# Kernel tuning notes

Hardware: AMD Instinct MI355X
Metric: run time of the kernel (lower is better)

## Reference

```python
import jax, jax.numpy as jnp
import numpy as np

T, N = 20, 32768          # seq_length, numNodes
D_IN, D_EMB, D_H, D_OUT = 2, 64, 128, 5


def setup_inputs() -> dict:
    key = jax.random.key(0)
    ks = jax.random.split(key, 12)
    s = 0.05
    return {
        "nodes": jax.random.normal(ks[0], (T, N, D_IN), jnp.float32),
        "present_mask": jax.random.randint(ks[1], (T, N), 0, 2).astype(bool),
        "hidden_states": jax.random.normal(ks[2], (N, D_H), jnp.float32),
        "cell_states": jax.random.normal(ks[3], (N, D_H), jnp.float32),
        "W_embed": jax.random.normal(ks[4], (D_IN, D_EMB), jnp.float32) * s,
        "b_embed": jnp.zeros((D_EMB,), jnp.float32),
        "W_ih": jax.random.normal(ks[5], (D_EMB, 4 * D_H), jnp.float32) * s,
        "b_ih": jnp.zeros((4 * D_H,), jnp.float32),
        "W_hh": jax.random.normal(ks[6], (D_H, 4 * D_H), jnp.float32) * s,
        "b_hh": jnp.zeros((4 * D_H,), jnp.float32),
        "W_out": jax.random.normal(ks[7], (D_H, D_OUT), jnp.float32) * s,
        "b_out": jnp.zeros((D_OUT,), jnp.float32),
    }


def reference(nodes, present_mask, hidden_states, cell_states,
              W_embed, b_embed, W_ih, b_ih, W_hh, b_hh, W_out, b_out):
    # Per-frame: gather present nodes -> embed+ReLU (dropout=eval identity)
    # -> LSTMCell -> scatter h/c/output back. Gather+scatter is expressed as
    # a masked update, which is mathematically identical.
    def step(carry, frame):
        h, c = carry
        x, mask = frame                      # x: [N,2], mask: [N]
        emb = jax.nn.relu(x @ W_embed + b_embed)              # [N,Demb]
        gates = emb @ W_ih + b_ih + h @ W_hh + b_hh           # [N,4H]
        i, f, g, o = jnp.split(gates, 4, axis=-1)             # torch order
        i, f, o = jax.nn.sigmoid(i), jax.nn.sigmoid(f), jax.nn.sigmoid(o)
        g = jnp.tanh(g)
        c_new = f * c + i * g
        h_new = o * jnp.tanh(c_new)
        m = mask[:, None]
        h = jnp.where(m, h_new, h)
        c = jnp.where(m, c_new, c)
        out = jnp.where(m, h_new @ W_out + b_out, 0.0)        # absent -> zeros
        return (h, c), out

    (h_fin, c_fin), outputs = jax.lax.scan(
        step, (hidden_states, cell_states), (nodes, present_mask))
    return outputs, h_fin, c_fin                              # [T,N,5],[N,H],[N,H]
```

## Files before the change

### kernel.cpp

```cpp
#include <hip/hip_runtime.h>
#include <cstddef>


typedef __attribute__((ext_vector_type(8))) short  s16x8;
typedef __attribute__((ext_vector_type(4))) float  f32x4;

namespace {
constexpr int T_STEPS = 20;
constexpr int NN      = 32768;
constexpr int D_EMB   = 64;
constexpr int D_H     = 128;
constexpr int D_OUT   = 5;
constexpr int G4      = 512;
constexpr int MT      = 64;
constexpr int BLOCK   = 512;
constexpr int GRID    = NN / MT;
constexpr int WP_ELEMS   = 8 * 4 * 6 * 64 * 8;
constexpr int WOUT_ELEMS = 4 * 64 * 8;
constexpr size_t OFF_H = (size_t)T_STEPS * NN * D_OUT;
constexpr size_t OFF_C = OFF_H + (size_t)NN * D_H;
}

__device__ __forceinline__ unsigned short f2bf(float x) {
    unsigned u = __float_as_uint(x);
    u = (u + 0x7FFFu + ((u >> 16) & 1u)) >> 16;
    return (unsigned short)u;
}
__device__ __forceinline__ float bf2f(unsigned short h) {
    return __uint_as_float(((unsigned)h) << 16);
}
__device__ __forceinline__ float sigf(float x) {
    return __builtin_amdgcn_rcpf(1.0f + __expf(-x));
}
__device__ __forceinline__ float tanhf_fast(float x) {
    return fmaf(-2.0f, __builtin_amdgcn_rcpf(1.0f + __expf(2.0f * x)), 1.0f);
}

__global__ void prepack_kernel(const float* __restrict__ W_ih,
                               const float* __restrict__ b_ih,
                               const float* __restrict__ W_hh,
                               const float* __restrict__ b_hh,
                               const float* __restrict__ W_out,
                               unsigned short* __restrict__ Wp,
                               unsigned short* __restrict__ WoutF,
                               float* __restrict__ b_sum) {
    int idx = blockIdx.x * blockDim.x + threadIdx.x;
    if (idx < WP_ELEMS) {
        int j    = idx & 7;
        int L    = (idx >> 3) & 63;
        int rest = idx >> 9;
        int kb   = rest % 6;
        int gw   = rest / 6;
        int g    = gw & 3, w = gw >> 2;
        int k    = kb * 32 + (L >> 4) * 8 + j;
        int col  = g * D_H + w * 16 + (L & 15);
        float v  = (k < D_EMB) ? W_ih[k * G4 + col] : W_hh[(k - D_EMB) * G4 + col];
        Wp[idx] = f2bf(v);
    } else if (idx < WP_ELEMS + WOUT_ELEMS) {
        int i2 = idx - WP_ELEMS;
        int j = i2 & 7, L = (i2 >> 3) & 63, kb2 = i2 >> 9;
        int k = kb2 * 32 + (L >> 4) * 8 + j;
        int n = L & 15;
        WoutF[i2] = (n < D_OUT) ? f2bf(W_out[k * D_OUT + n]) : (unsigned short)0;
    }
    if (idx < G4) b_sum[idx] = b_ih[idx] + b_hh[idx];
}

__global__ __launch_bounds__(BLOCK, 2) void vlstm_kernel(
    const float* __restrict__ nodes,
    const int*   __restrict__ mask,
    const float* __restrict__ h0,
    const float* __restrict__ c0,
    const float* __restrict__ W_embed,
    const float* __restrict__ b_embed,
    const float* __restrict__ b_out,
    const unsigned short* __restrict__ Wp,
    const unsigned short* __restrict__ WoutF,
    const float* __restrict__ b_sum,
    float* __restrict__ out)
{
    __shared__ __align__(16) unsigned short A[24 * 64 * 8];
    __shared__ __align__(16) float st_out[MT * D_OUT];
    __shared__ float We_s[2 * D_EMB];
    __shared__ float be_s[D_EMB];
    __shared__ int   msk_s[2][MT];

    const int tid  = threadIdx.x;
    const int wave = tid >> 6;
    const int L    = tid & 63;
    const int quad = L >> 4;
    const int l15  = L & 15;
    const int n_base = blockIdx.x * MT;

    const unsigned short* wbase = Wp + (size_t)wave * (4 * 6 * 64 * 8);
    s16x8 Bf[4][6];
    #pragma unroll
    for (int g = 0; g < 4; g++)
        #pragma unroll
        for (int kb = 0; kb < 6; kb++)
            Bf[g][kb] = *(const s16x8*)(wbase + ((g * 6 + kb) * 64 + L) * 8);
    s16x8 WoF[4];
    #pragma unroll
    for (int kb2 = 0; kb2 < 4; kb2++)
        WoF[kb2] = *(const s16x8*)(WoutF + ((kb2 * 64) + L) * 8);

    float bias[4];
    #pragma unroll
    for (int g = 0; g < 4; g++) bias[g] = b_sum[g * D_H + wave * 16 + l15];
    const float bo = (l15 < D_OUT) ? b_out[l15] : 0.0f;

    for (int i = tid; i < 3 * D_EMB; i += BLOCK) {
        if (i < 2 * D_EMB) We_s[i] = W_embed[i];
        else               be_s[i - 2 * D_EMB] = b_embed[i - 2 * D_EMB];
    }
    for (int i = tid; i < MT * D_H; i += BLOCK) {
        int node = i >> 7, u = i & 127;
        int k = D_EMB + u;
        int idx = (((node >> 4) * 6 + (k >> 5)) * 64 + ((k >> 3) & 3) * 16 + (node & 15)) * 8 + (k & 7);
        A[idx] = f2bf(h0[(size_t)(n_base + node) * D_H + u]);
    }
    const int u_lane = wave * 16 + l15;
    float c[4][4];
    #pragma unroll
    for (int rt = 0; rt < 4; rt++)
        #pragma unroll
        for (int r = 0; r < 4; r++) {
            int m = rt * 16 + quad * 4 + r;
            c[rt][r] = c0[(size_t)(n_base + m) * D_H + u_lane];
        }
    __syncthreads();

    const int node_e = tid >> 3;
    const int eb     = tid & 7;

    {
        const float2* xp = (const float2*)(nodes + ((size_t)0 * NN + n_base + node_e) * 2);
        float2 x = *xp;
        s16x8 ev;
        #pragma unroll
        for (int j = 0; j < 8; j++) {
            int e = eb * 8 + j;
            float v = fmaf(x.x, We_s[e], fmaf(x.y, We_s[D_EMB + e], be_s[e]));
            ev[j] = (short)f2bf(fmaxf(v, 0.0f));
        }
        int idx = (((node_e >> 4) * 6 + (eb >> 2)) * 64 + (eb & 3) * 16 + (node_e & 15)) * 8;
        *(s16x8*)(A + idx) = ev;
        if (tid < MT) msk_s[0][tid] = mask[(size_t)0 * NN + n_base + tid];
    }
    __syncthreads();

    for (int t = 0; t < T_STEPS; t++) {
        f32x4 acc[4][4];
        #pragma unroll
        for (int rt = 0; rt < 4; rt++)
            #pragma unroll
            for (int g = 0; g < 4; g++)
                acc[rt][g] = (f32x4){bias[g], bias[g], bias[g], bias[g]};
        #pragma unroll
        for (int kb = 0; kb < 6; kb++) {
            #pragma unroll
            for (int rt = 0; rt < 4; rt++) {
                s16x8 af = *(const s16x8*)(A + ((rt * 6 + kb) * 64 + L) * 8);
                #pragma unroll
                for (int g = 0; g < 4; g++)
                    acc[rt][g] = __builtin_amdgcn_mfma_f32_16x16x32_bf16(
                        af, Bf[g][kb], acc[rt][g], 0, 0, 0);
            }
        }

        unsigned mbits = 0;
        unsigned short hbf[4][4];
        #pragma unroll
        for (int rt = 0; rt < 4; rt++)
            #pragma unroll
            for (int r = 0; r < 4; r++) {
                int m = rt * 16 + quad * 4 + r;
                int mval = msk_s[t & 1][m];
                float gi = sigf(acc[rt][0][r]);
                float gf = sigf(acc[rt][1][r]);
                float gg = tanhf_fast(acc[rt][2][r]);
                float go = sigf(acc[rt][3][r]);
                float cn = fmaf(gf, c[rt][r], gi * gg);
                float hv = go * tanhf_fast(cn);
                if (mval) { c[rt][r] = cn; mbits |= 1u << (rt * 4 + r); }
                hbf[rt][r] = f2bf(hv);
            }
        __syncthreads();

        if (t > 0 && tid < MT * D_OUT)
            out[((size_t)(t - 1) * NN + n_base) * D_OUT + tid] = st_out[tid];

        {
            int kb_u = 2 + (u_lane >> 5);
            int fl   = ((u_lane >> 3) & 3) * 16 + quad * 4;
            int j_u  = u_lane & 7;
            #pragma unroll
            for (int rt = 0; rt < 4; rt++)
                #pragma unroll
                for (int r = 0; r < 4; r++)
                    if ((mbits >> (rt * 4 + r)) & 1u)
                        A[((rt * 6 + kb_u) * 64 + fl + r) * 8 + j_u] = hbf[rt][r];
        }
        if (t + 1 < T_STEPS) {
            const float2* xp = (const float2*)(nodes + ((size_t)(t + 1) * NN + n_base + node_e) * 2);
            float2 x = *xp;
            s16x8 ev;
            #pragma unroll
            for (int j = 0; j < 8; j++) {
                int e = eb * 8 + j;
                float v = fmaf(x.x, We_s[e], fmaf(x.y, We_s[D_EMB + e], be_s[e]));
                ev[j] = (short)f2bf(fmaxf(v, 0.0f));
            }
            int idx = (((node_e >> 4) * 6 + (eb >> 2)) * 64 + (eb & 3) * 16 + (node_e & 15)) * 8;
            *(s16x8*)(A + idx) = ev;
            if (tid < MT) msk_s[(t + 1) & 1][tid] = mask[(size_t)(t + 1) * NN + n_base + tid];
        }
        __syncthreads();

        if (wave < 4) {
            const int rt = wave;
            f32x4 ao = (f32x4){0.0f, 0.0f, 0.0f, 0.0f};
            #pragma unroll
            for (int kb2 = 0; kb2 < 4; kb2++) {
                s16x8 af = *(const s16x8*)(A + ((rt * 6 + 2 + kb2) * 64 + L) * 8);
                ao = __builtin_amdgcn_mfma_f32_16x16x32_bf16(af, WoF[kb2], ao, 0, 0, 0);
            }
            if (l15 < D_OUT) {
                #pragma unroll
                for (int r = 0; r < 4; r++) {
                    int node = rt * 16 + quad * 4 + r;
                    int mv = msk_s[t & 1][node];
                    st_out[node * D_OUT + l15] = mv ? (ao[r] + bo) : 0.0f;
                }
            }
        }
    }

    __syncthreads();
    if (tid < MT * D_OUT)
        out[((size_t)(T_STEPS - 1) * NN + n_base) * D_OUT + tid] = st_out[tid];

    for (int i = tid; i < MT * D_H; i += BLOCK) {
        int node = i >> 7, u = i & 127;
        int k = D_EMB + u;
        int idx = (((node >> 4) * 6 + (k >> 5)) * 64 + ((k >> 3) & 3) * 16 + (node & 15)) * 8 + (k & 7);
        out[OFF_H + (size_t)(n_base + node) * D_H + u] = bf2f(A[idx]);
    }
    #pragma unroll
    for (int rt = 0; rt < 4; rt++)
        #pragma unroll
        for (int r = 0; r < 4; r++) {
            int m = rt * 16 + quad * 4 + r;
            out[OFF_C + (size_t)(n_base + m) * D_H + u_lane] = c[rt][r];
        }
}

extern "C" void kernel_launch(void* const* d_in, const int* in_sizes, int n_in,
                              void* d_out, int out_size, void* d_ws, size_t ws_size,
                              hipStream_t stream) {
    const float* nodes   = (const float*)d_in[0];
    const int*   mask    = (const int*)  d_in[1];
    const float* h0      = (const float*)d_in[2];
    const float* c0      = (const float*)d_in[3];
    const float* W_embed = (const float*)d_in[4];
    const float* b_embed = (const float*)d_in[5];
    const float* W_ih    = (const float*)d_in[6];
    const float* b_ih    = (const float*)d_in[7];
    const float* W_hh    = (const float*)d_in[8];
    const float* b_hh    = (const float*)d_in[9];
    const float* W_out   = (const float*)d_in[10];
    const float* b_out   = (const float*)d_in[11];
    float* out = (float*)d_out;

    unsigned short* Wp    = (unsigned short*)d_ws;
    unsigned short* WoutF = Wp + WP_ELEMS;
    float*          b_sum = (float*)(WoutF + WOUT_ELEMS);

    prepack_kernel<<<(WP_ELEMS + WOUT_ELEMS + 255) / 256, 256, 0, stream>>>(
        W_ih, b_ih, W_hh, b_hh, W_out, Wp, WoutF, b_sum);

    vlstm_kernel<<<GRID, BLOCK, 0, stream>>>(
        nodes, mask, h0, c0, W_embed, b_embed, b_out, Wp, WoutF, b_sum, out);
}
```

Measured before the change: 331.3 us.

## Double-buffer LDS activation tile to cut one barrier per LSTM step

The single shared A tile becomes two ping-pong buffers, so each step reads the current buffer and writes h and the next embedding into the other, leaving one __syncthreads per step instead of two. The output projection for step k-1 and the global store for step k-2 are moved to the start of step k, overlapping with the gate matmul. Next-step inputs and the mask are loaded early into registers to hide global latency, and h is now kept in registers and written in full each step. In exchange, LDS use roughly doubles, which may cut occupancy at 2 blocks per CU, and register pressure goes up.

```diff
diff --git a/kernel.cpp b/kernel.cpp
--- a/kernel.cpp
+++ b/kernel.cpp
@@ -17,6 +17,7 @@
 constexpr int GRID    = NN / MT;
 constexpr int WP_ELEMS   = 8 * 4 * 6 * 64 * 8;
 constexpr int WOUT_ELEMS = 4 * 64 * 8;
+constexpr int AELEMS  = 24 * 64 * 8;
 constexpr size_t OFF_H = (size_t)T_STEPS * NN * D_OUT;
 constexpr size_t OFF_C = OFF_H + (size_t)NN * D_H;
 }
@@ -79,8 +80,8 @@
     const float* __restrict__ b_sum,
     float* __restrict__ out)
 {
-    __shared__ __align__(16) unsigned short A[24 * 64 * 8];
-    __shared__ __align__(16) float st_out[MT * D_OUT];
+    __shared__ __align__(16) unsigned short Abuf[2][AELEMS];
+    __shared__ __align__(16) float st_out[2][MT * D_OUT];
     __shared__ float We_s[2 * D_EMB];
     __shared__ float be_s[D_EMB];
     __shared__ int   msk_s[2][MT];
@@ -117,18 +118,19 @@
         int node = i >> 7, u = i & 127;
         int k = D_EMB + u;
         int idx = (((node >> 4) * 6 + (k >> 5)) * 64 + ((k >> 3) & 3) * 16 + (node & 15)) * 8 + (k & 7);
-        A[idx] = f2bf(h0[(size_t)(n_base + node) * D_H + u]);
+        Abuf[0][idx] = f2bf(h0[(size_t)(n_base + node) * D_H + u]);
     }
     const int u_lane = wave * 16 + l15;
     float c[4][4];
+    unsigned short hcur[4][4];
     #pragma unroll
     for (int rt = 0; rt < 4; rt++)
         #pragma unroll
         for (int r = 0; r < 4; r++) {
             int m = rt * 16 + quad * 4 + r;
-            c[rt][r] = c0[(size_t)(n_base + m) * D_H + u_lane];
-        }
-    __syncthreads();
+            c[rt][r]    = c0[(size_t)(n_base + m) * D_H + u_lane];
+            hcur[rt][r] = f2bf(h0[(size_t)(n_base + m) * D_H + u_lane]);
+        }
 
     const int node_e = tid >> 3;
     const int eb     = tid & 7;
@@ -144,12 +146,51 @@
             ev[j] = (short)f2bf(fmaxf(v, 0.0f));
         }
         int idx = (((node_e >> 4) * 6 + (eb >> 2)) * 64 + (eb & 3) * 16 + (node_e & 15)) * 8;
-        *(s16x8*)(A + idx) = ev;
+        *(s16x8*)(Abuf[0] + idx) = ev;
         if (tid < MT) msk_s[0][tid] = mask[(size_t)0 * NN + n_base + tid];
     }
     __syncthreads();
 
-    for (int t = 0; t < T_STEPS; t++) {
+    const int kb_u = 2 + (u_lane >> 5);
+    const int fl   = ((u_lane >> 3) & 3) * 16 + quad * 4;
+    const int j_u  = u_lane & 7;
+
+    unsigned mprev = 0;
+
+    for (int k = 0; k < T_STEPS; k++) {
+        const int p = k & 1;
+        const unsigned short* Ac = Abuf[p];
+        unsigned short*       An = Abuf[1 - p];
+        const bool has_next = (k + 1 < T_STEPS);
+
+        float2 xv = {0.0f, 0.0f};
+        int mpf = 0;
+        if (has_next) {
+            xv = *(const float2*)(nodes + ((size_t)(k + 1) * NN + n_base + node_e) * 2);
+            if (tid < MT) mpf = mask[(size_t)(k + 1) * NN + n_base + tid];
+        }
+
+        if (k > 0 && wave < 4) {
+            const int rt = wave;
+            f32x4 ao = (f32x4){0.0f, 0.0f, 0.0f, 0.0f};
+            #pragma unroll
+            for (int kb2 = 0; kb2 < 4; kb2++) {
+                s16x8 af = *(const s16x8*)(Ac + ((rt * 6 + 2 + kb2) * 64 + L) * 8);
+                ao = __builtin_amdgcn_mfma_f32_16x16x32_bf16(af, WoF[kb2], ao, 0, 0, 0);
+            }
+            if (l15 < D_OUT) {
+                #pragma unroll
+                for (int r = 0; r < 4; r++) {
+                    int node = rt * 16 + quad * 4 + r;
+                    st_out[1 - p][node * D_OUT + l15] =
+                        ((mprev >> (rt * 4 + r)) & 1u) ? (ao[r] + bo) : 0.0f;
+                }
+            }
+        }
+
+        if (k > 1 && tid < MT * D_OUT)
+            out[((size_t)(k - 2) * NN + n_base) * D_OUT + tid] = st_out[p][tid];
+
         f32x4 acc[4][4];
         #pragma unroll
         for (int rt = 0; rt < 4; rt++)
@@ -160,7 +201,7 @@
         for (int kb = 0; kb < 6; kb++) {
             #pragma unroll
             for (int rt = 0; rt < 4; rt++) {
-                s16x8 af = *(const s16x8*)(A + ((rt * 6 + kb) * 64 + L) * 8);
+                s16x8 af = *(const s16x8*)(Ac + ((rt * 6 + kb) * 64 + L) * 8);
                 #pragma unroll
                 for (int g = 0; g < 4; g++)
                     acc[rt][g] = __builtin_amdgcn_mfma_f32_16x16x32_bf16(
@@ -169,82 +210,84 @@
         }
 
         unsigned mbits = 0;
-        unsigned short hbf[4][4];
         #pragma unroll
         for (int rt = 0; rt < 4; rt++)
             #pragma unroll
             for (int r = 0; r < 4; r++) {
                 int m = rt * 16 + quad * 4 + r;
-                int mval = msk_s[t & 1][m];
+                int mval = msk_s[p][m];
                 float gi = sigf(acc[rt][0][r]);
                 float gf = sigf(acc[rt][1][r]);
                 float gg = tanhf_fast(acc[rt][2][r]);
                 float go = sigf(acc[rt][3][r]);
                 float cn = fmaf(gf, c[rt][r], gi * gg);
                 float hv = go * tanhf_fast(cn);
-                if (mval) { c[rt][r] = cn; mbits |= 1u << (rt * 4 + r); }
-                hbf[rt][r] = f2bf(hv);
-            }
-        __syncthreads();
-
-        if (t > 0 && tid < MT * D_OUT)
-            out[((size_t)(t - 1) * NN + n_base) * D_OUT + tid] = st_out[tid];
-
-        {
-            int kb_u = 2 + (u_lane >> 5);
-            int fl   = ((u_lane >> 3) & 3) * 16 + quad * 4;
-            int j_u  = u_lane & 7;
-            #pragma unroll
-            for (int rt = 0; rt < 4; rt++)
-                #pragma unroll
-                for (int r = 0; r < 4; r++)
-                    if ((mbits >> (rt * 4 + r)) & 1u)
-                        A[((rt * 6 + kb_u) * 64 + fl + r) * 8 + j_u] = hbf[rt][r];
-        }
-        if (t + 1 < T_STEPS) {
-            const float2* xp = (const float2*)(nodes + ((size_t)(t + 1) * NN + n_base + node_e) * 2);
-            float2 x = *xp;
+                if (mval) {
+                    c[rt][r]    = cn;
+                    hcur[rt][r] = f2bf(hv);
+                    mbits |= 1u << (rt * 4 + r);
+                }
+            }
+        mprev = mbits;
+
+        #pragma unroll
+        for (int rt = 0; rt < 4; rt++)
+            #pragma unroll
+            for (int r = 0; r < 4; r++)
+                An[((rt * 6 + kb_u) * 64 + fl + r) * 8 + j_u] = hcur[rt][r];
+
+        if (has_next) {
             s16x8 ev;
             #pragma unroll
             for (int j = 0; j < 8; j++) {
                 int e = eb * 8 + j;
-                float v = fmaf(x.x, We_s[e], fmaf(x.y, We_s[D_EMB + e], be_s[e]));
+                float v = fmaf(xv.x, We_s[e], fmaf(xv.y, We_s[D_EMB + e], be_s[e]));
                 ev[j] = (short)f2bf(fmaxf(v, 0.0f));
             }
             int idx = (((node_e >> 4) * 6 + (eb >> 2)) * 64 + (eb & 3) * 16 + (node_e & 15)) * 8;
-            *(s16x8*)(A + idx) = ev;
-            if (tid < MT) msk_s[(t + 1) & 1][tid] = mask[(size_t)(t + 1) * NN + n_base + tid];
-        }
+            *(s16x8*)(An + idx) = ev;
+            if (tid < MT) msk_s[1 - p][tid] = mpf;
+        }
+
         __syncthreads();
-
+    }
+
+    {
+        const unsigned short* Ah = Abuf[T_STEPS & 1];
         if (wave < 4) {
             const int rt = wave;
             f32x4 ao = (f32x4){0.0f, 0.0f, 0.0f, 0.0f};
             #pragma unroll
             for (int kb2 = 0; kb2 < 4; kb2++) {
-                s16x8 af = *(const s16x8*)(A + ((rt * 6 + 2 + kb2) * 64 + L) * 8);
+                s16x8 af = *(const s16x8*)(Ah + ((rt * 6 + 2 + kb2) * 64 + L) * 8);
                 ao = __builtin_amdgcn_mfma_f32_16x16x32_bf16(af, WoF[kb2], ao, 0, 0, 0);
             }
             if (l15 < D_OUT) {
                 #pragma unroll
                 for (int r = 0; r < 4; r++) {
                     int node = rt * 16 + quad * 4 + r;
-                    int mv = msk_s[t & 1][node];
-                    st_out[node * D_OUT + l15] = mv ? (ao[r] + bo) : 0.0f;
+                    st_out[(T_STEPS - 1) & 1][node * D_OUT + l15] =
+                        ((mprev >> (rt * 4 + r)) & 1u) ? (ao[r] + bo) : 0.0f;
                 }
             }
         }
-    }
-
+        if (tid < MT * D_OUT)
+            out[((size_t)(T_STEPS - 2) * NN + n_base) * D_OUT + tid] =
+                st_out[(T_STEPS - 2) & 1][tid];
+    }
     __syncthreads();
     if (tid < MT * D_OUT)
-        out[((size_t)(T_STEPS - 1) * NN + n_base) * D_OUT + tid] = st_out[tid];
-
-    for (int i = tid; i < MT * D_H; i += BLOCK) {
-        int node = i >> 7, u = i & 127;
-        int k = D_EMB + u;
-        int idx = (((node >> 4) * 6 + (k >> 5)) * 64 + ((k >> 3) & 3) * 16 + (node & 15)) * 8 + (k & 7);
-        out[OFF_H + (size_t)(n_base + node) * D_H + u] = bf2f(A[idx]);
+        out[((size_t)(T_STEPS - 1) * NN + n_base) * D_OUT + tid] =
+            st_out[(T_STEPS - 1) & 1][tid];
+
+    {
+        const unsigned short* Ah = Abuf[T_STEPS & 1];
+        for (int i = tid; i < MT * D_H; i += BLOCK) {
+            int node = i >> 7, u = i & 127;
+            int kk = D_EMB + u;
+            int idx = (((node >> 4) * 6 + (kk >> 5)) * 64 + ((kk >> 3) & 3) * 16 + (node & 15)) * 8 + (kk & 7);
+            out[OFF_H + (size_t)(n_base + node) * D_H + u] = bf2f(Ah[idx]);
+        }
     }
     #pragma unroll
     for (int rt = 0; rt < 4; rt++)
```

Result: slower. 401.6 us (+21.2%).

## Double node tile per block and prefetch next-step inputs before MFMA

Applied to the files above, without the earlier changes.

Doubles the node tile per block from 64 to 128, so each wave reuses its register-resident gate weights across 8 row tiles, processed in two halves. Next-frame node coordinates and mask are loaded into registers before the gate MFMAs to hide global latency. The output projection weights move from registers to LDS so all 8 waves can do the output MFMA, and the output mask is taken from the per-lane mask bits. bf16 packing now uses paired conversions. The risks are a grid of only 256 blocks, which lowers occupancy, and higher register pressure that could cause spills.

```diff
diff --git a/kernel.cpp b/kernel.cpp
--- a/kernel.cpp
+++ b/kernel.cpp
@@ -1,4 +1,5 @@
 #include <hip/hip_runtime.h>
+#include <hip/hip_bf16.h>
 #include <cstddef>
 
 
@@ -12,11 +13,12 @@
 constexpr int D_H     = 128;
 constexpr int D_OUT   = 5;
 constexpr int G4      = 512;
-constexpr int MT      = 64;
+constexpr int MT      = 128;
 constexpr int BLOCK   = 512;
 constexpr int GRID    = NN / MT;
 constexpr int WP_ELEMS   = 8 * 4 * 6 * 64 * 8;
 constexpr int WOUT_ELEMS = 4 * 64 * 8;
+constexpr int AELEMS  = 8 * 6 * 64 * 8;
 constexpr size_t OFF_H = (size_t)T_STEPS * NN * D_OUT;
 constexpr size_t OFF_C = OFF_H + (size_t)NN * D_H;
 }
@@ -28,6 +30,10 @@
 }
 __device__ __forceinline__ float bf2f(unsigned short h) {
     return __uint_as_float(((unsigned)h) << 16);
+}
+__device__ __forceinline__ unsigned pk2bf(float lo, float hi) {
+    __hip_bfloat162 p = __float22bfloat162_rn(make_float2(lo, hi));
+    return *(unsigned*)&p;
 }
 __device__ __forceinline__ float sigf(float x) {
     return __builtin_amdgcn_rcpf(1.0f + __expf(-x));
@@ -79,7 +85,8 @@
     const float* __restrict__ b_sum,
     float* __restrict__ out)
 {
-    __shared__ __align__(16) unsigned short A[24 * 64 * 8];
+    __shared__ __align__(16) unsigned short A[AELEMS];
+    __shared__ __align__(16) unsigned short WoF_s[WOUT_ELEMS];
     __shared__ __align__(16) float st_out[MT * D_OUT];
     __shared__ float We_s[2 * D_EMB];
     __shared__ float be_s[D_EMB];
@@ -99,16 +106,14 @@
         #pragma unroll
         for (int kb = 0; kb < 6; kb++)
             Bf[g][kb] = *(const s16x8*)(wbase + ((g * 6 + kb) * 64 + L) * 8);
-    s16x8 WoF[4];
-    #pragma unroll
-    for (int kb2 = 0; kb2 < 4; kb2++)
-        WoF[kb2] = *(const s16x8*)(WoutF + ((kb2 * 64) + L) * 8);
 
     float bias[4];
     #pragma unroll
     for (int g = 0; g < 4; g++) bias[g] = b_sum[g * D_H + wave * 16 + l15];
     const float bo = (l15 < D_OUT) ? b_out[l15] : 0.0f;
 
+    for (int i = tid; i < WOUT_ELEMS / 8; i += BLOCK)
+        *(s16x8*)(WoF_s + i * 8) = *(const s16x8*)(WoutF + i * 8);
     for (int i = tid; i < 3 * D_EMB; i += BLOCK) {
         if (i < 2 * D_EMB) We_s[i] = W_embed[i];
         else               be_s[i - 2 * D_EMB] = b_embed[i - 2 * D_EMB];
@@ -120,125 +125,152 @@
         A[idx] = f2bf(h0[(size_t)(n_base + node) * D_H + u]);
     }
     const int u_lane = wave * 16 + l15;
-    float c[4][4];
+    float c[8][4];
     #pragma unroll
-    for (int rt = 0; rt < 4; rt++)
+    for (int rt = 0; rt < 8; rt++)
         #pragma unroll
         for (int r = 0; r < 4; r++) {
             int m = rt * 16 + quad * 4 + r;
             c[rt][r] = c0[(size_t)(n_base + m) * D_H + u_lane];
         }
-    __syncthreads();
 
     const int node_e = tid >> 3;
     const int eb     = tid & 7;
 
     {
-        const float2* xp = (const float2*)(nodes + ((size_t)0 * NN + n_base + node_e) * 2);
-        float2 x = *xp;
-        s16x8 ev;
-        #pragma unroll
-        for (int j = 0; j < 8; j++) {
-            int e = eb * 8 + j;
-            float v = fmaf(x.x, We_s[e], fmaf(x.y, We_s[D_EMB + e], be_s[e]));
-            ev[j] = (short)f2bf(fmaxf(v, 0.0f));
-        }
-        int idx = (((node_e >> 4) * 6 + (eb >> 2)) * 64 + (eb & 3) * 16 + (node_e & 15)) * 8;
-        *(s16x8*)(A + idx) = ev;
+        #pragma unroll
+        for (int h = 0; h < 2; h++) {
+            int node = node_e + 64 * h;
+            float2 x = *(const float2*)(nodes + ((size_t)0 * NN + n_base + node) * 2);
+            union { s16x8 v; unsigned u[4]; } ev;
+            #pragma unroll
+            for (int jp = 0; jp < 4; jp++) {
+                int e = eb * 8 + jp * 2;
+                float v0 = fmaf(x.x, We_s[e],     fmaf(x.y, We_s[D_EMB + e],     be_s[e]));
+                float v1 = fmaf(x.x, We_s[e + 1], fmaf(x.y, We_s[D_EMB + e + 1], be_s[e + 1]));
+                ev.u[jp] = pk2bf(fmaxf(v0, 0.0f), fmaxf(v1, 0.0f));
+            }
+            int idx = (((node >> 4) * 6 + (eb >> 2)) * 64 + (eb & 3) * 16 + (node & 15)) * 8;
+            *(s16x8*)(A + idx) = ev.v;
+        }
         if (tid < MT) msk_s[0][tid] = mask[(size_t)0 * NN + n_base + tid];
     }
     __syncthreads();
 
+    const int kb_u = 2 + (u_lane >> 5);
+    const int fl   = ((u_lane >> 3) & 3) * 16 + quad * 4;
+    const int j_u  = u_lane & 7;
+
     for (int t = 0; t < T_STEPS; t++) {
-        f32x4 acc[4][4];
-        #pragma unroll
-        for (int rt = 0; rt < 4; rt++)
-            #pragma unroll
-            for (int g = 0; g < 4; g++)
-                acc[rt][g] = (f32x4){bias[g], bias[g], bias[g], bias[g]};
-        #pragma unroll
-        for (int kb = 0; kb < 6; kb++) {
-            #pragma unroll
-            for (int rt = 0; rt < 4; rt++) {
-                s16x8 af = *(const s16x8*)(A + ((rt * 6 + kb) * 64 + L) * 8);
+        const int p = t & 1;
+        const bool has_next = (t + 1 < T_STEPS);
+
+        float2 xv[2] = {{0.f, 0.f}, {0.f, 0.f}};
+        int mpf = 0;
+        if (has_next) {
+            xv[0] = *(const float2*)(nodes + ((size_t)(t + 1) * NN + n_base + node_e) * 2);
+            xv[1] = *(const float2*)(nodes + ((size_t)(t + 1) * NN + n_base + node_e + 64) * 2);
+            if (tid < MT) mpf = mask[(size_t)(t + 1) * NN + n_base + tid];
+        }
+
+        unsigned mbits = 0;
+        unsigned hpk[8][2];
+        #pragma unroll
+        for (int half = 0; half < 2; half++) {
+            f32x4 acc[4][4];
+            #pragma unroll
+            for (int q = 0; q < 4; q++)
                 #pragma unroll
                 for (int g = 0; g < 4; g++)
-                    acc[rt][g] = __builtin_amdgcn_mfma_f32_16x16x32_bf16(
-                        af, Bf[g][kb], acc[rt][g], 0, 0, 0);
-            }
-        }
-
-        unsigned mbits = 0;
-        unsigned short hbf[4][4];
-        #pragma unroll
-        for (int rt = 0; rt < 4; rt++)
-            #pragma unroll
-            for (int r = 0; r < 4; r++) {
-                int m = rt * 16 + quad * 4 + r;
-                int mval = msk_s[t & 1][m];
-                float gi = sigf(acc[rt][0][r]);
-                float gf = sigf(acc[rt][1][r]);
-                float gg = tanhf_fast(acc[rt][2][r]);
-                float go = sigf(acc[rt][3][r]);
-                float cn = fmaf(gf, c[rt][r], gi * gg);
-                float hv = go * tanhf_fast(cn);
-                if (mval) { c[rt][r] = cn; mbits |= 1u << (rt * 4 + r); }
-                hbf[rt][r] = f2bf(hv);
-            }
+                    acc[q][g] = (f32x4){bias[g], bias[g], bias[g], bias[g]};
+            #pragma unroll
+            for (int kb = 0; kb < 6; kb++) {
+                #pragma unroll
+                for (int q = 0; q < 4; q++) {
+                    int rt = half * 4 + q;
+                    s16x8 af = *(const s16x8*)(A + ((rt * 6 + kb) * 64 + L) * 8);
+                    #pragma unroll
+                    for (int g = 0; g < 4; g++)
+                        acc[q][g] = __builtin_amdgcn_mfma_f32_16x16x32_bf16(
+                            af, Bf[g][kb], acc[q][g], 0, 0, 0);
+                }
+            }
+            #pragma unroll
+            for (int q = 0; q < 4; q++) {
+                int rt = half * 4 + q;
+                float hv[4];
+                #pragma unroll
+                for (int r = 0; r < 4; r++) {
+                    int m = rt * 16 + quad * 4 + r;
+                    int mval = msk_s[p][m];
+                    float gi = sigf(acc[q][0][r]);
+                    float gf = sigf(acc[q][1][r]);
+                    float gg = tanhf_fast(acc[q][2][r]);
+                    float go = sigf(acc[q][3][r]);
+                    float cn = fmaf(gf, c[rt][r], gi * gg);
+                    hv[r] = go * tanhf_fast(cn);
+                    if (mval) { c[rt][r] = cn; mbits |= 1u << (rt * 4 + r); }
+                }
+                hpk[rt][0] = pk2bf(hv[0], hv[1]);
+                hpk[rt][1] = pk2bf(hv[2], hv[3]);
+            }
+        }
         __syncthreads();
 
-        if (t > 0 && tid < MT * D_OUT)
-            out[((size_t)(t - 1) * NN + n_base) * D_OUT + tid] = st_out[tid];
+        if (t > 0)
+            for (int i = tid; i < MT * D_OUT; i += BLOCK)
+                out[((size_t)(t - 1) * NN + n_base) * D_OUT + i] = st_out[i];
+
+        #pragma unroll
+        for (int rt = 0; rt < 8; rt++)
+            #pragma unroll
+            for (int r = 0; r < 4; r++)
+                if ((mbits >> (rt * 4 + r)) & 1u)
+                    A[((rt * 6 + kb_u) * 64 + fl + r) * 8 + j_u] =
+                        (unsigned short)(hpk[rt][r >> 1] >> ((r & 1) * 16));
+
+        if (has_next) {
+            #pragma unroll
+            for (int h = 0; h < 2; h++) {
+                int node = node_e + 64 * h;
+                union { s16x8 v; unsigned u[4]; } ev;
+                #pragma unroll
+                for (int jp = 0; jp < 4; jp++) {
+                    int e = eb * 8 + jp * 2;
+                    float v0 = fmaf(xv[h].x, We_s[e],     fmaf(xv[h].y, We_s[D_EMB + e],     be_s[e]));
+                    float v1 = fmaf(xv[h].x, We_s[e + 1], fmaf(xv[h].y, We_s[D_EMB + e + 1], be_s[e + 1]));
+                    ev.u[jp] = pk2bf(fmaxf(v0, 0.0f), fmaxf(v1, 0.0f));
+                }
+                int idx = (((node >> 4) * 6 + (eb >> 2)) * 64 + (eb & 3) * 16 + (node & 15)) * 8;
+                *(s16x8*)(A + idx) = ev.v;
+            }
+            if (tid < MT) msk_s[1 - p][tid] = mpf;
+        }
+        __syncthreads();
 
         {
-            int kb_u = 2 + (u_lane >> 5);
-            int fl   = ((u_lane >> 3) & 3) * 16 + quad * 4;
-            int j_u  = u_lane & 7;
-            #pragma unroll
-            for (int rt = 0; rt < 4; rt++)
-                #pragma unroll
-                for (int r = 0; r < 4; r++)
-                    if ((mbits >> (rt * 4 + r)) & 1u)
-                        A[((rt * 6 + kb_u) * 64 + fl + r) * 8 + j_u] = hbf[rt][r];
-        }
-        if (t + 1 < T_STEPS) {
-            const float2* xp = (const float2*)(nodes + ((size_t)(t + 1) * NN + n_base + node_e) * 2);
-            float2 x = *xp;
-            s16x8 ev;
-            #pragma unroll
-            for (int j = 0; j < 8; j++) {
-                int e = eb * 8 + j;
-                float v = fmaf(x.x, We_s[e], fmaf(x.y, We_s[D_EMB + e], be_s[e]));
-                ev[j] = (short)f2bf(fmaxf(v, 0.0f));
-            }
-            int idx = (((node_e >> 4) * 6 + (eb >> 2)) * 64 + (eb & 3) * 16 + (node_e & 15)) * 8;
-            *(s16x8*)(A + idx) = ev;
-            if (tid < MT) msk_s[(t + 1) & 1][tid] = mask[(size_t)(t + 1) * NN + n_base + tid];
-        }
-        __syncthreads();
-
-        if (wave < 4) {
             const int rt = wave;
             f32x4 ao = (f32x4){0.0f, 0.0f, 0.0f, 0.0f};
             #pragma unroll
             for (int kb2 = 0; kb2 < 4; kb2++) {
                 s16x8 af = *(const s16x8*)(A + ((rt * 6 + 2 + kb2) * 64 + L) * 8);
-                ao = __builtin_amdgcn_mfma_f32_16x16x32_bf16(af, WoF[kb2], ao, 0, 0, 0);
+                s16x8 wf = *(const s16x8*)(WoF_s + (kb2 * 64 + L) * 8);
+                ao = __builtin_amdgcn_mfma_f32_16x16x32_bf16(af, wf, ao, 0, 0, 0);
             }
             if (l15 < D_OUT) {
                 #pragma unroll
                 for (int r = 0; r < 4; r++) {
                     int node = rt * 16 + quad * 4 + r;
-                    int mv = msk_s[t & 1][node];
-                    st_out[node * D_OUT + l15] = mv ? (ao[r] + bo) : 0.0f;
+                    st_out[node * D_OUT + l15] =
+                        ((mbits >> (rt * 4 + r)) & 1u) ? (ao[r] + bo) : 0.0f;
                 }
             }
         }
     }
 
     __syncthreads();
-    if (tid < MT * D_OUT)
-        out[((size_t)(T_STEPS - 1) * NN + n_base) * D_OUT + tid] = st_out[tid];
+    for (int i = tid; i < MT * D_OUT; i += BLOCK)
+        out[((size_t)(T_STEPS - 1) * NN + n_base) * D_OUT + i] = st_out[i];
 
     for (int i = tid; i < MT * D_H; i += BLOCK) {
         int node = i >> 7, u = i & 127;
@@ -247,7 +279,7 @@
         out[OFF_H + (size_t)(n_base + node) * D_H + u] = bf2f(A[idx]);
     }
     #pragma unroll
-    for (int rt = 0; rt < 4; rt++)
+    for (int rt = 0; rt < 8; rt++)
         #pragma unroll
         for (int r = 0; r < 4; r++) {
             int m = rt * 16 + quad * 4 + r;
```

Measured after the change: 550.7 us. 66.2% more time.

## Split LSTM gates across wave pairs with LDS exchange, double block size

Applied to the files above, without the earlier changes.

Doubles the block to 1024 threads (16 waves). Each pair of waves now shares a 16-unit slice, with each wave computing two of the four gates. The odd wave applies the g/o activations and passes them as packed bf16 through a new LDS exchange buffer. The even wave finishes the cell update and writes h back. This halves per-wave MFMA and register work so more waves can overlap, and next-step input loads are now issued before the matmul. In exchange it adds a synchronized LDS round trip, bf16 rounding of the g/o activations, and heavier LDS use that may limit occupancy.

```diff
diff --git a/kernel.cpp b/kernel.cpp
--- a/kernel.cpp
+++ b/kernel.cpp
@@ -1,4 +1,5 @@
 #include <hip/hip_runtime.h>
+#include <hip/hip_bf16.h>
 #include <cstddef>
 
 
@@ -13,10 +14,11 @@
 constexpr int D_OUT   = 5;
 constexpr int G4      = 512;
 constexpr int MT      = 64;
-constexpr int BLOCK   = 512;
+constexpr int BLOCK   = 1024;
 constexpr int GRID    = NN / MT;
-constexpr int WP_ELEMS   = 8 * 4 * 6 * 64 * 8;
+constexpr int WP_ELEMS   = 16 * 2 * 6 * 64 * 8;
 constexpr int WOUT_ELEMS = 4 * 64 * 8;
+constexpr int AELEMS  = 24 * 64 * 8;
 constexpr size_t OFF_H = (size_t)T_STEPS * NN * D_OUT;
 constexpr size_t OFF_C = OFF_H + (size_t)NN * D_H;
 }
@@ -28,6 +30,10 @@
 }
 __device__ __forceinline__ float bf2f(unsigned short h) {
     return __uint_as_float(((unsigned)h) << 16);
+}
+__device__ __forceinline__ unsigned pk2bf(float lo, float hi) {
+    __hip_bfloat162 p = __float22bfloat162_rn(make_float2(lo, hi));
+    return *(unsigned*)&p;
 }
 __device__ __forceinline__ float sigf(float x) {
     return __builtin_amdgcn_rcpf(1.0f + __expf(-x));
@@ -50,10 +56,12 @@
         int L    = (idx >> 3) & 63;
         int rest = idx >> 9;
         int kb   = rest % 6;
-        int gw   = rest / 6;
-        int g    = gw & 3, w = gw >> 2;
+        int wg   = rest / 6;
+        int gg   = wg & 1, w = wg >> 1;
+        int ug   = w >> 1;
+        int gate = (w & 1) * 2 + gg;
         int k    = kb * 32 + (L >> 4) * 8 + j;
-        int col  = g * D_H + w * 16 + (L & 15);
+        int col  = gate * D_H + ug * 16 + (L & 15);
         float v  = (k < D_EMB) ? W_ih[k * G4 + col] : W_hh[(k - D_EMB) * G4 + col];
         Wp[idx] = f2bf(v);
     } else if (idx < WP_ELEMS + WOUT_ELEMS) {
@@ -66,7 +74,7 @@
     if (idx < G4) b_sum[idx] = b_ih[idx] + b_hh[idx];
 }
 
-__global__ __launch_bounds__(BLOCK, 2) void vlstm_kernel(
+__global__ __launch_bounds__(BLOCK, 4) void vlstm_kernel(
     const float* __restrict__ nodes,
     const int*   __restrict__ mask,
     const float* __restrict__ h0,
@@ -79,7 +87,8 @@
     const float* __restrict__ b_sum,
     float* __restrict__ out)
 {
-    __shared__ __align__(16) unsigned short A[24 * 64 * 8];
+    __shared__ __align__(16) unsigned short A[AELEMS];
+    __shared__ __align__(16) unsigned Xex[8 * 64 * 17];
     __shared__ __align__(16) float st_out[MT * D_OUT];
     __shared__ float We_s[2 * D_EMB];
     __shared__ float be_s[D_EMB];
@@ -87,26 +96,34 @@
 
     const int tid  = threadIdx.x;
     const int wave = tid >> 6;
+    const int aodd = wave & 1;
+    const int ug   = wave >> 1;
     const int L    = tid & 63;
     const int quad = L >> 4;
     const int l15  = L & 15;
     const int n_base = blockIdx.x * MT;
-
-    const unsigned short* wbase = Wp + (size_t)wave * (4 * 6 * 64 * 8);
-    s16x8 Bf[4][6];
+    const int u_lane = ug * 16 + l15;
+
+    const unsigned short* wbase = Wp + (size_t)wave * (2 * 6 * 64 * 8);
+    s16x8 Bf[2][6];
     #pragma unroll
-    for (int g = 0; g < 4; g++)
+    for (int gg = 0; gg < 2; gg++)
         #pragma unroll
         for (int kb = 0; kb < 6; kb++)
-            Bf[g][kb] = *(const s16x8*)(wbase + ((g * 6 + kb) * 64 + L) * 8);
+            Bf[gg][kb] = *(const s16x8*)(wbase + ((gg * 6 + kb) * 64 + L) * 8);
+
+    float bias[2];
+    #pragma unroll
+    for (int gg = 0; gg < 2; gg++)
+        bias[gg] = b_sum[(aodd * 2 + gg) * D_H + u_lane];
+
     s16x8 WoF[4];
-    #pragma unroll
-    for (int kb2 = 0; kb2 < 4; kb2++)
-        WoF[kb2] = *(const s16x8*)(WoutF + ((kb2 * 64) + L) * 8);
-
-    float bias[4];
-    #pragma unroll
-    for (int g = 0; g < 4; g++) bias[g] = b_sum[g * D_H + wave * 16 + l15];
+    const int do_oproj = (aodd == 1 && ug < 4);
+    if (do_oproj) {
+        #pragma unroll
+        for (int kb2 = 0; kb2 < 4; kb2++)
+            WoF[kb2] = *(const s16x8*)(WoutF + ((kb2 * 64) + L) * 8);
+    }
     const float bo = (l15 < D_OUT) ? b_out[l15] : 0.0f;
 
     for (int i = tid; i < 3 * D_EMB; i += BLOCK) {
@@ -119,106 +136,124 @@
         int idx = (((node >> 4) * 6 + (k >> 5)) * 64 + ((k >> 3) & 3) * 16 + (node & 15)) * 8 + (k & 7);
         A[idx] = f2bf(h0[(size_t)(n_base + node) * D_H + u]);
     }
-    const int u_lane = wave * 16 + l15;
     float c[4][4];
-    #pragma unroll
-    for (int rt = 0; rt < 4; rt++)
-        #pragma unroll
-        for (int r = 0; r < 4; r++) {
-            int m = rt * 16 + quad * 4 + r;
-            c[rt][r] = c0[(size_t)(n_base + m) * D_H + u_lane];
-        }
+    if (aodd == 0) {
+        #pragma unroll
+        for (int rt = 0; rt < 4; rt++)
+            #pragma unroll
+            for (int r = 0; r < 4; r++) {
+                int m = rt * 16 + quad * 4 + r;
+                c[rt][r] = c0[(size_t)(n_base + m) * D_H + u_lane];
+            }
+    }
+
+    const int node_e = tid >> 4;
+    const int eb     = tid & 15;
+
+    {
+        float2 x = *(const float2*)(nodes + ((size_t)0 * NN + n_base + node_e) * 2);
+        int e0 = eb * 4;
+        float v0 = fmaf(x.x, We_s[e0],     fmaf(x.y, We_s[D_EMB + e0],     be_s[e0]));
+        float v1 = fmaf(x.x, We_s[e0 + 1], fmaf(x.y, We_s[D_EMB + e0 + 1], be_s[e0 + 1]));
+        float v2 = fmaf(x.x, We_s[e0 + 2], fmaf(x.y, We_s[D_EMB + e0 + 2], be_s[e0 + 2]));
+        float v3 = fmaf(x.x, We_s[e0 + 3], fmaf(x.y, We_s[D_EMB + e0 + 3], be_s[e0 + 3]));
+        uint2 pk;
+        pk.x = pk2bf(fmaxf(v0, 0.0f), fmaxf(v1, 0.0f));
+        pk.y = pk2bf(fmaxf(v2, 0.0f), fmaxf(v3, 0.0f));
+        int idx = (((node_e >> 4) * 6 + (e0 >> 5)) * 64 + ((e0 >> 3) & 3) * 16 + (node_e & 15)) * 8 + (e0 & 7);
+        *(uint2*)(A + idx) = pk;
+        if (tid < MT) msk_s[0][tid] = mask[(size_t)0 * NN + n_base + tid];
+    }
     __syncthreads();
 
-    const int node_e = tid >> 3;
-    const int eb     = tid & 7;
-
-    {
-        const float2* xp = (const float2*)(nodes + ((size_t)0 * NN + n_base + node_e) * 2);
-        float2 x = *xp;
-        s16x8 ev;
-        #pragma unroll
-        for (int j = 0; j < 8; j++) {
-            int e = eb * 8 + j;
-            float v = fmaf(x.x, We_s[e], fmaf(x.y, We_s[D_EMB + e], be_s[e]));
-            ev[j] = (short)f2bf(fmaxf(v, 0.0f));
-        }
-        int idx = (((node_e >> 4) * 6 + (eb >> 2)) * 64 + (eb & 3) * 16 + (node_e & 15)) * 8;
-        *(s16x8*)(A + idx) = ev;
-        if (tid < MT) msk_s[0][tid] = mask[(size_t)0 * NN + n_base + tid];
-    }
-    __syncthreads();
+    const int kb_u = 2 + (u_lane >> 5);
+    const int fl   = ((u_lane >> 3) & 3) * 16 + quad * 4;
+    const int j_u  = u_lane & 7;
+    const int xbase = (ug * 64 + L) * 17;
 
     for (int t = 0; t < T_STEPS; t++) {
-        f32x4 acc[4][4];
+        const int p = t & 1;
+        const bool has_next = (t + 1 < T_STEPS);
+
+        float2 xv = {0.0f, 0.0f};
+        int mpf = 0;
+        if (has_next) {
+            xv = *(const float2*)(nodes + ((size_t)(t + 1) * NN + n_base + node_e) * 2);
+            if (tid < MT) mpf = mask[(size_t)(t + 1) * NN + n_base + tid];
+        }
+
+        f32x4 acc[4][2];
         #pragma unroll
         for (int rt = 0; rt < 4; rt++)
             #pragma unroll
-            for (int g = 0; g < 4; g++)
-                acc[rt][g] = (f32x4){bias[g], bias[g], bias[g], bias[g]};
+            for (int gg = 0; gg < 2; gg++)
+                acc[rt][gg] = (f32x4){bias[gg], bias[gg], bias[gg], bias[gg]};
         #pragma unroll
         for (int kb = 0; kb < 6; kb++) {
             #pragma unroll
             for (int rt = 0; rt < 4; rt++) {
                 s16x8 af = *(const s16x8*)(A + ((rt * 6 + kb) * 64 + L) * 8);
-                #pragma unroll
-                for (int g = 0; g < 4; g++)
-                    acc[rt][g] = __builtin_amdgcn_mfma_f32_16x16x32_bf16(
-                        af, Bf[g][kb], acc[rt][g], 0, 0, 0);
-            }
-        }
-
-        unsigned mbits = 0;
-        unsigned short hbf[4][4];
-        #pragma unroll
-        for (int rt = 0; rt < 4; rt++)
-            #pragma unroll
-            for (int r = 0; r < 4; r++) {
-                int m = rt * 16 + quad * 4 + r;
-                int mval = msk_s[t & 1][m];
-                float gi = sigf(acc[rt][0][r]);
-                float gf = sigf(acc[rt][1][r]);
-                float gg = tanhf_fast(acc[rt][2][r]);
-                float go = sigf(acc[rt][3][r]);
-                float cn = fmaf(gf, c[rt][r], gi * gg);
-                float hv = go * tanhf_fast(cn);
-                if (mval) { c[rt][r] = cn; mbits |= 1u << (rt * 4 + r); }
-                hbf[rt][r] = f2bf(hv);
-            }
+                acc[rt][0] = __builtin_amdgcn_mfma_f32_16x16x32_bf16(af, Bf[0][kb], acc[rt][0], 0, 0, 0);
+                acc[rt][1] = __builtin_amdgcn_mfma_f32_16x16x32_bf16(af, Bf[1][kb], acc[rt][1], 0, 0, 0);
+            }
+        }
+
+        if (aodd == 1) {
+            #pragma unroll
+            for (int rt = 0; rt < 4; rt++) {
+                uint4 xw;
+                xw.x = pk2bf(tanhf_fast(acc[rt][0][0]), sigf(acc[rt][1][0]));
+                xw.y = pk2bf(tanhf_fast(acc[rt][0][1]), sigf(acc[rt][1][1]));
+                xw.z = pk2bf(tanhf_fast(acc[rt][0][2]), sigf(acc[rt][1][2]));
+                xw.w = pk2bf(tanhf_fast(acc[rt][0][3]), sigf(acc[rt][1][3]));
+                *(uint4*)(Xex + xbase + rt * 4) = xw;
+            }
+        }
         __syncthreads();
 
         if (t > 0 && tid < MT * D_OUT)
             out[((size_t)(t - 1) * NN + n_base) * D_OUT + tid] = st_out[tid];
 
-        {
-            int kb_u = 2 + (u_lane >> 5);
-            int fl   = ((u_lane >> 3) & 3) * 16 + quad * 4;
-            int j_u  = u_lane & 7;
-            #pragma unroll
-            for (int rt = 0; rt < 4; rt++)
+        if (aodd == 0) {
+            #pragma unroll
+            for (int rt = 0; rt < 4; rt++) {
+                uint4 xr = *(const uint4*)(Xex + xbase + rt * 4);
+                unsigned xa[4] = {xr.x, xr.y, xr.z, xr.w};
                 #pragma unroll
-                for (int r = 0; r < 4; r++)
-                    if ((mbits >> (rt * 4 + r)) & 1u)
-                        A[((rt * 6 + kb_u) * 64 + fl + r) * 8 + j_u] = hbf[rt][r];
-        }
-        if (t + 1 < T_STEPS) {
-            const float2* xp = (const float2*)(nodes + ((size_t)(t + 1) * NN + n_base + node_e) * 2);
-            float2 x = *xp;
-            s16x8 ev;
-            #pragma unroll
-            for (int j = 0; j < 8; j++) {
-                int e = eb * 8 + j;
-                float v = fmaf(x.x, We_s[e], fmaf(x.y, We_s[D_EMB + e], be_s[e]));
-                ev[j] = (short)f2bf(fmaxf(v, 0.0f));
-            }
-            int idx = (((node_e >> 4) * 6 + (eb >> 2)) * 64 + (eb & 3) * 16 + (node_e & 15)) * 8;
-            *(s16x8*)(A + idx) = ev;
-            if (tid < MT) msk_s[(t + 1) & 1][tid] = mask[(size_t)(t + 1) * NN + n_base + tid];
+                for (int r = 0; r < 4; r++) {
+                    int m = rt * 16 + quad * 4 + r;
+                    int mval = msk_s[p][m];
+                    float si = sigf(acc[rt][0][r]);
+                    float sf = sigf(acc[rt][1][r]);
+                    float tg = bf2f((unsigned short)(xa[r] & 0xFFFFu));
+                    float so = bf2f((unsigned short)(xa[r] >> 16));
+                    float cn = fmaf(sf, c[rt][r], si * tg);
+                    float hv = so * tanhf_fast(cn);
+                    if (mval) {
+                        c[rt][r] = cn;
+                        A[((rt * 6 + kb_u) * 64 + fl + r) * 8 + j_u] = f2bf(hv);
+                    }
+                }
+            }
+        }
+
+        if (has_next) {
+            int e0 = eb * 4;
+            float v0 = fmaf(xv.x, We_s[e0],     fmaf(xv.y, We_s[D_EMB + e0],     be_s[e0]));
+            float v1 = fmaf(xv.x, We_s[e0 + 1], fmaf(xv.y, We_s[D_EMB + e0 + 1], be_s[e0 + 1]));
+            float v2 = fmaf(xv.x, We_s[e0 + 2], fmaf(xv.y, We_s[D_EMB + e0 + 2], be_s[e0 + 2]));
+            float v3 = fmaf(xv.x, We_s[e0 + 3], fmaf(xv.y, We_s[D_EMB + e0 + 3], be_s[e0 + 3]));
+            uint2 pk;
+            pk.x = pk2bf(fmaxf(v0, 0.0f), fmaxf(v1, 0.0f));
+            pk.y = pk2bf(fmaxf(v2, 0.0f), fmaxf(v3, 0.0f));
+            int idx = (((node_e >> 4) * 6 + (e0 >> 5)) * 64 + ((e0 >> 3) & 3) * 16 + (node_e & 15)) * 8 + (e0 & 7);
+            *(uint2*)(A + idx) = pk;
+            if (tid < MT) msk_s[1 - p][tid] = mpf;
         }
         __syncthreads();
 
-        if (wave < 4) {
-            const int rt = wave;
+        if (do_oproj) {
+            const int rt = ug;
             f32x4 ao = (f32x4){0.0f, 0.0f, 0.0f, 0.0f};
             #pragma unroll
             for (int kb2 = 0; kb2 < 4; kb2++) {
@@ -229,8 +264,8 @@
                 #pragma unroll
                 for (int r = 0; r < 4; r++) {
                     int node = rt * 16 + quad * 4 + r;
-                    int mv = msk_s[t & 1][node];
-                    st_out[node * D_OUT + l15] = mv ? (ao[r] + bo) : 0.0f;
+                    st_out[node * D_OUT + l15] =
+                        msk_s[p][node] ? (ao[r] + bo) : 0.0f;
                 }
             }
         }
@@ -246,13 +281,15 @@
         int idx = (((node >> 4) * 6 + (k >> 5)) * 64 + ((k >> 3) & 3) * 16 + (node & 15)) * 8 + (k & 7);
         out[OFF_H + (size_t)(n_base + node) * D_H + u] = bf2f(A[idx]);
     }
-    #pragma unroll
-    for (int rt = 0; rt < 4; rt++)
-        #pragma unroll
-        for (int r = 0; r < 4; r++) {
-            int m = rt * 16 + quad * 4 + r;
-            out[OFF_C + (size_t)(n_base + m) * D_H + u_lane] = c[rt][r];
-        }
+    if (aodd == 0) {
+        #pragma unroll
+        for (int rt = 0; rt < 4; rt++)
+            #pragma unroll
+            for (int r = 0; r < 4; r++) {
+                int m = rt * 16 + quad * 4 + r;
+                out[OFF_C + (size_t)(n_base + m) * D_H + u_lane] = c[rt][r];
+            }
+    }
 }
 
 extern "C" void kernel_launch(void* const* d_in, const int* in_sizes, int n_in,
```

Result: slower. 509.9 us (+53.9%).
